# Kernel tuning notes

Measured on AMD Instinct MI355X. Metric: run time of the kernel, lower is better.

## Reference

```python
import jax, jax.numpy as jnp
import numpy as np

COUNT_BINS = 8
BOUND = 3.0
MIN_BIN_WIDTH = 1e-3
MIN_BIN_HEIGHT = 1e-3
MIN_DERIVATIVE = 1e-3
EPS = 1e-6


def _made_masks(D, H1, H2, M):
    indeg = np.arange(1, D + 1)                     # input degrees 1..D
    h1 = np.arange(H1) % (D - 1) + 1                # hidden degrees in [1, D-1]
    h2 = np.arange(H2) % (D - 1) + 1
    outdeg = np.tile(indeg, M)                      # (M*D,), reshape-compatible with (M, D)
    m1 = (h1[:, None] >= indeg[None, :]).astype(np.float32)   # (H1, D)
    m2 = (h2[:, None] >= h1[None, :]).astype(np.float32)      # (H2, H1)
    m3 = (outdeg[:, None] > h2[None, :]).astype(np.float32)   # (M*D, H2)
    return jnp.asarray(m1), jnp.asarray(m2), jnp.asarray(m3)


def _rq_spline_forward(x, w, h, d):
    # x: (B, D); w, h: (B, D, K) simplex weights; d: (B, D, K-1) softplus'd interior derivatives
    K = w.shape[-1]
    left, right = -BOUND, BOUND

    widths = MIN_BIN_WIDTH + (1.0 - MIN_BIN_WIDTH * K) * w
    heights = MIN_BIN_HEIGHT + (1.0 - MIN_BIN_HEIGHT * K) * h
    derivs = MIN_DERIVATIVE + d
    ones = jnp.ones_like(derivs[..., :1])
    derivs = jnp.concatenate([ones, derivs, ones], -1)          # (B, D, K+1), boundary slope 1

    cw = jnp.cumsum(widths, -1)
    edge_l = jnp.full_like(cw[..., :1], left)
    edge_r = jnp.full_like(cw[..., :1], right)
    cumw = jnp.concatenate([edge_l, left + (right - left) * cw[..., :-1], edge_r], -1)  # (B, D, K+1)
    widths = cumw[..., 1:] - cumw[..., :-1]
    ch = jnp.cumsum(heights, -1)
    cumh = jnp.concatenate([edge_l, left + (right - left) * ch[..., :-1], edge_r], -1)
    heights = cumh[..., 1:] - cumh[..., :-1]

    inside = (x >= left) & (x <= right)
    xc = jnp.clip(x, left, right)
    # pyro: bin_idx = sum(x >= cumwidths + eps) - 1
    idx = jnp.sum((xc[..., None] >= (cumw + EPS)).astype(jnp.int32), -1) - 1
    idx = jnp.clip(idx, 0, K - 1)                               # (B, D)

    def g(t):
        return jnp.take_along_axis(t, idx[..., None], axis=-1)[..., 0]

    x_k, w_k = g(cumw), g(widths)
    y_k, h_k = g(cumh), g(heights)
    delta = h_k / w_k
    d_k, d_k1 = g(derivs), g(derivs[..., 1:])

    theta = (xc - x_k) / w_k
    tt = theta * (1.0 - theta)
    num = h_k * (delta * theta ** 2 + d_k * tt)
    den = delta + (d_k + d_k1 - 2.0 * delta) * tt
    y = y_k + num / den
    dnum = delta ** 2 * (d_k1 * theta ** 2 + 2.0 * delta * tt + d_k * (1.0 - theta) ** 2)
    ld = jnp.log(dnum) - 2.0 * jnp.log(den)
    return jnp.where(inside, y, x), jnp.where(inside, ld, jnp.zeros_like(ld))


def _forward(x, W1, b1, W2, b2, W3, b3):
    B, D = x.shape
    H1, H2 = W1.shape[0], W2.shape[0]
    K = COUNT_BINS
    M = 3 * K - 1
    m1, m2, m3 = _made_masks(D, H1, H2, M)
    h1 = jax.nn.relu(x @ (W1 * m1).T + b1)
    h2 = jax.nn.relu(h1 @ (W2 * m2).T + b2)
    p = (h2 @ (W3 * m3).T + b3).reshape(B, M, D)                # (B, 3K-1, D)
    w = jax.nn.softmax(jnp.swapaxes(p[:, :K, :], 1, 2), axis=-1)          # (B, D, K)
    hgt = jax.nn.softmax(jnp.swapaxes(p[:, K:2 * K, :], 1, 2), axis=-1)   # (B, D, K)
    d = jax.nn.softplus(jnp.swapaxes(p[:, 2 * K:, :], 1, 2))              # (B, D, K-1)
    z, ld = _rq_spline_forward(x, w, hgt, d)
    return z, ld.sum(-1)


def setup_inputs() -> dict:
    key = jax.random.key(0)
    ks = jax.random.split(key, 7)
    B, D, H1, H2 = 32768, 64, 64, 32
    M = 3 * COUNT_BINS - 1
    s1, s2, s3 = 1.0 / np.sqrt(D), 1.0 / np.sqrt(H1), 1.0 / np.sqrt(H2)
    return {
        "x": jax.random.normal(ks[0], (B, D), jnp.float32),
        "W1": jax.random.uniform(ks[1], (H1, D), jnp.float32, -s1, s1),
        "b1": jax.random.uniform(ks[2], (H1,), jnp.float32, -s1, s1),
        "W2": jax.random.uniform(ks[3], (H2, H1), jnp.float32, -s2, s2),
        "b2": jax.random.uniform(ks[4], (H2,), jnp.float32, -s2, s2),
        "W3": jax.random.uniform(ks[5], (M * D, H2), jnp.float32, -s3, s3),
        "b3": jax.random.uniform(ks[6], (M * D,), jnp.float32, -s3, s3),
    }


def reference(x, W1, b1, W2, b2, W3, b3):
    return _forward(x, W1, b1, W2, b2, W3, b3)
```

## Files before the change

kernel.cpp:

```cpp
#include <hip/hip_runtime.h>

#define NM 23

typedef short short8 __attribute__((ext_vector_type(8)));
typedef float f32x4 __attribute__((ext_vector_type(4)));

#define LOG2E 1.44269504088896340736f

__device__ __forceinline__ float softplus_f(float v) {
  return fmaxf(v, 0.f) + __logf(1.f + __expf(-fabsf(v)));
}

__device__ __forceinline__ float fastrcp(float v) {
  return __builtin_amdgcn_rcpf(v);
}

__device__ __forceinline__ unsigned short bf16_rne(float x) {
  unsigned u = __float_as_uint(x);
  u += 0x7FFFu + ((u >> 16) & 1u);
  return (unsigned short)(u >> 16);
}

__global__ __launch_bounds__(256) void prep_kernel(
    const float* __restrict__ W1, const float* __restrict__ W2,
    const float* __restrict__ W3,
    unsigned short* __restrict__ B1hi, unsigned short* __restrict__ B1lo,
    unsigned short* __restrict__ B2hi, unsigned short* __restrict__ B2lo,
    unsigned short* __restrict__ B3hi, unsigned short* __restrict__ B3lo) {
  const int idx = blockIdx.x * 256 + threadIdx.x;
  const int j = idx & 7, lane = (idx >> 3) & 63;
  const int col = lane & 15, quad = lane >> 4;

  if (idx < 4096) {
    const int rest = idx >> 9, kt = rest & 1, nt = rest >> 1;
    const int k = kt * 32 + quad * 8 + j;
    const int n = nt * 16 + col;
    const float v = ((n % 63) >= k) ? W1[n * 64 + k] : 0.f;
    const unsigned short h = bf16_rne(v);
    B1hi[idx] = h;
    B1lo[idx] = bf16_rne(v - __uint_as_float(((unsigned)h) << 16));
  }
  if (idx < 2048) {
    const int rest = idx >> 9, kt = rest & 1, nt = rest >> 1;
    const int k = kt * 32 + quad * 8 + j;
    const int n = nt * 16 + col;
    const float v = ((k % 63) <= n) ? W2[n * 64 + k] : 0.f;
    const unsigned short h = bf16_rne(v);
    B2hi[idx] = h;
    B2lo[idx] = bf16_rne(v - __uint_as_float(((unsigned)h) << 16));
  }
  if (idx < 92 * 64 * 8) {
    const int nt = idx >> 9;
    const int n = nt * 16 + col;
    const int d = n & 63;
    const int m = n >> 6;
    const int k = quad * 8 + j;
    float v = (k < d) ? W3[(size_t)n * 32 + k] : 0.f;
    if (m < 16) v *= LOG2E;
    const unsigned short h = bf16_rne(v);
    B3hi[idx] = h;
    B3lo[idx] = bf16_rne(v - __uint_as_float(((unsigned)h) << 16));
  }
}

__device__ __forceinline__ void cvt_hilo(const float* src, short8& hi,
                                         short8& lo) {
  const f32x4 a0 = *reinterpret_cast<const f32x4*>(src);
  const f32x4 a1 = *reinterpret_cast<const f32x4*>(src + 4);
  const float af[8] = {a0.x, a0.y, a0.z, a0.w, a1.x, a1.y, a1.z, a1.w};
  #pragma unroll
  for (int j = 0; j < 8; ++j) {
    const unsigned short h = bf16_rne(af[j]);
    hi[j] = (short)h;
    lo[j] = (short)bf16_rne(af[j] - __uint_as_float(((unsigned)h) << 16));
  }
}

__global__ __launch_bounds__(512, 4) void fused_kernel(
    const float* __restrict__ x,
    const unsigned short* __restrict__ B1hi,
    const unsigned short* __restrict__ B1lo,
    const float* __restrict__ b1,
    const unsigned short* __restrict__ B2hi,
    const unsigned short* __restrict__ B2lo,
    const float* __restrict__ b2,
    const unsigned short* __restrict__ B3hi,
    const unsigned short* __restrict__ B3lo,
    const float* __restrict__ b3,
    float* __restrict__ out, int B) {
  __shared__ float h1s[32][68];
  __shared__ float h2s[32][68];
  __shared__ float b3s[64 * NM];
  __shared__ float ldp[4][32];

  const int t = threadIdx.x;
  const int b0 = blockIdx.x * 32;

  for (int idx = t; idx < 64 * NM; idx += 512) {
    const int dl = idx / NM, m = idx - dl * NM;
    const float s = (m < 16) ? LOG2E : 1.f;
    b3s[idx] = b3[m * 64 + dl] * s;
  }
  __syncthreads();

  const int lane = t & 63;
  const int wv   = __builtin_amdgcn_readfirstlane(t >> 6);
  const int col  = lane & 15;
  const int quad = lane >> 4;

  {
    const int mt1 = wv >> 2, nt1 = wv & 3;
    const float* xrow = x + (size_t)(b0 + mt1 * 16 + col) * 64;
    short8 ahi[2], alo[2];
    #pragma unroll
    for (int kt = 0; kt < 2; ++kt)
      cvt_hilo(xrow + kt * 32 + quad * 8, ahi[kt], alo[kt]);

    const float bv = b1[nt1 * 16 + col];
    f32x4 acc = {bv, bv, bv, bv};
    #pragma unroll
    for (int kt = 0; kt < 2; ++kt) {
      const size_t off = ((size_t)(nt1 * 2 + kt) * 64 + lane) * 8;
      const short8 bh = *reinterpret_cast<const short8*>(B1hi + off);
      const short8 bl = *reinterpret_cast<const short8*>(B1lo + off);
      acc = __builtin_amdgcn_mfma_f32_16x16x32_bf16(ahi[kt], bh, acc, 0, 0, 0);
      acc = __builtin_amdgcn_mfma_f32_16x16x32_bf16(alo[kt], bh, acc, 0, 0, 0);
      acc = __builtin_amdgcn_mfma_f32_16x16x32_bf16(ahi[kt], bl, acc, 0, 0, 0);
    }
    #pragma unroll
    for (int reg = 0; reg < 4; ++reg)
      h1s[mt1 * 16 + quad * 4 + reg][nt1 * 16 + col] = fmaxf(acc[reg], 0.f);
  }
  __syncthreads();

  if (wv < 4) {
    const int mt2 = wv >> 1, nt2 = wv & 1;
    short8 ahi[2], alo[2];
    #pragma unroll
    for (int kt = 0; kt < 2; ++kt)
      cvt_hilo(&h1s[mt2 * 16 + col][kt * 32 + quad * 8], ahi[kt], alo[kt]);

    const float bv = b2[nt2 * 16 + col];
    f32x4 acc = {bv, bv, bv, bv};
    #pragma unroll
    for (int kt = 0; kt < 2; ++kt) {
      const size_t off = ((size_t)(nt2 * 2 + kt) * 64 + lane) * 8;
      const short8 bh = *reinterpret_cast<const short8*>(B2hi + off);
      const short8 bl = *reinterpret_cast<const short8*>(B2lo + off);
      acc = __builtin_amdgcn_mfma_f32_16x16x32_bf16(ahi[kt], bh, acc, 0, 0, 0);
      acc = __builtin_amdgcn_mfma_f32_16x16x32_bf16(alo[kt], bh, acc, 0, 0, 0);
      acc = __builtin_amdgcn_mfma_f32_16x16x32_bf16(ahi[kt], bl, acc, 0, 0, 0);
    }
    #pragma unroll
    for (int reg = 0; reg < 4; ++reg)
      h2s[mt2 * 16 + quad * 4 + reg][nt2 * 16 + col] = fmaxf(acc[reg], 0.f);
  }
  __syncthreads();

  const int mt = wv >> 2, dc = wv & 3;
  const int row0 = mt * 16 + quad * 4;
  const int d = dc * 16 + col;

  short8 ahi, alo;
  cvt_hilo(&h2s[mt * 16 + col][quad * 8], ahi, alo);

  float xvv[4];
  #pragma unroll
  for (int reg = 0; reg < 4; ++reg)
    xvv[reg] = x[(size_t)(b0 + row0 + reg) * 64 + d];

  __syncthreads();

  float ldr[4] = {0.f, 0.f, 0.f, 0.f};
  const float WSC = 1.0f - 1e-3f * 8.0f;

  float xcv[4], fidx[4], xkv[4], wkv[4], ykv[4], hkv[4];

  {
    f32x4 acc[8];
    #pragma unroll
    for (int m = 0; m < 8; ++m) {
      const float bv = b3s[d * NM + m];
      acc[m] = (f32x4){bv, bv, bv, bv};
    }
    #pragma unroll
    for (int m = 0; m < 8; ++m) {
      const size_t off = ((size_t)(4 * m + dc) * 64 + lane) * 8;
      const short8 bh = *reinterpret_cast<const short8*>(B3hi + off);
      const short8 bl = *reinterpret_cast<const short8*>(B3lo + off);
      acc[m] = __builtin_amdgcn_mfma_f32_16x16x32_bf16(ahi, bh, acc[m], 0, 0, 0);
      acc[m] = __builtin_amdgcn_mfma_f32_16x16x32_bf16(alo, bh, acc[m], 0, 0, 0);
      acc[m] = __builtin_amdgcn_mfma_f32_16x16x32_bf16(ahi, bl, acc[m], 0, 0, 0);
    }
    #pragma unroll
    for (int reg = 0; reg < 4; ++reg) {
      float ew[8], sw = 0.f;
      #pragma unroll
      for (int k = 0; k < 8; ++k) { ew[k] = exp2f(acc[k][reg]); sw += ew[k]; }
      const float invw = fastrcp(sw);
      float cumw[9];
      cumw[0] = -3.f;
      float cw = 0.f;
      #pragma unroll
      for (int k = 0; k < 7; ++k) {
        cw += 1e-3f + WSC * (ew[k] * invw);
        cumw[k + 1] = fmaf(6.f, cw, -3.f);
      }
      cumw[8] = 3.f;

      const float xv = xvv[reg];
      const float xc = fminf(fmaxf(xv, -3.f), 3.f);
      float fi = 0.f, xk = cumw[0], xk1 = cumw[1];
      #pragma unroll
      for (int k = 1; k < 8; ++k) {
        const bool s = xc >= cumw[k] + 1e-6f;
        xk  = s ? cumw[k]     : xk;
        xk1 = s ? cumw[k + 1] : xk1;
        fi  = s ? (float)k    : fi;
      }
      xcv[reg] = xc; fidx[reg] = fi; xkv[reg] = xk; wkv[reg] = xk1 - xk;
    }
  }

  {
    f32x4 acc[8];
    #pragma unroll
    for (int m = 0; m < 8; ++m) {
      const float bv = b3s[d * NM + (8 + m)];
      acc[m] = (f32x4){bv, bv, bv, bv};
    }
    #pragma unroll
    for (int m = 0; m < 8; ++m) {
      const size_t off = ((size_t)(4 * (8 + m) + dc) * 64 + lane) * 8;
      const short8 bh = *reinterpret_cast<const short8*>(B3hi + off);
      const short8 bl = *reinterpret_cast<const short8*>(B3lo + off);
      acc[m] = __builtin_amdgcn_mfma_f32_16x16x32_bf16(ahi, bh, acc[m], 0, 0, 0);
      acc[m] = __builtin_amdgcn_mfma_f32_16x16x32_bf16(alo, bh, acc[m], 0, 0, 0);
      acc[m] = __builtin_amdgcn_mfma_f32_16x16x32_bf16(ahi, bl, acc[m], 0, 0, 0);
    }
    #pragma unroll
    for (int reg = 0; reg < 4; ++reg) {
      float eh[8], sh = 0.f;
      #pragma unroll
      for (int k = 0; k < 8; ++k) { eh[k] = exp2f(acc[k][reg]); sh += eh[k]; }
      const float invh = fastrcp(sh);
      float cumh[9];
      cumh[0] = -3.f;
      float ch = 0.f;
      #pragma unroll
      for (int k = 0; k < 7; ++k) {
        ch += 1e-3f + WSC * (eh[k] * invh);
        cumh[k + 1] = fmaf(6.f, ch, -3.f);
      }
      cumh[8] = 3.f;

      float yk = cumh[0], yk1 = cumh[1];
      #pragma unroll
      for (int k = 1; k < 8; ++k) {
        const bool s = fidx[reg] >= (float)k;
        yk  = s ? cumh[k]     : yk;
        yk1 = s ? cumh[k + 1] : yk1;
      }
      ykv[reg] = yk; hkv[reg] = yk1 - yk;
    }
  }

  {
    f32x4 acc[7];
    #pragma unroll
    for (int m = 0; m < 7; ++m) {
      const float bv = b3s[d * NM + (16 + m)];
      acc[m] = (f32x4){bv, bv, bv, bv};
    }
    #pragma unroll
    for (int m = 0; m < 7; ++m) {
      const size_t off = ((size_t)(4 * (16 + m) + dc) * 64 + lane) * 8;
      const short8 bh = *reinterpret_cast<const short8*>(B3hi + off);
      const short8 bl = *reinterpret_cast<const short8*>(B3lo + off);
      acc[m] = __builtin_amdgcn_mfma_f32_16x16x32_bf16(ahi, bh, acc[m], 0, 0, 0);
      acc[m] = __builtin_amdgcn_mfma_f32_16x16x32_bf16(alo, bh, acc[m], 0, 0, 0);
      acc[m] = __builtin_amdgcn_mfma_f32_16x16x32_bf16(ahi, bl, acc[m], 0, 0, 0);
    }
    #pragma unroll
    for (int reg = 0; reg < 4; ++reg) {
      float p[7];
      #pragma unroll
      for (int k = 0; k < 7; ++k) p[k] = acc[k][reg];
      const float fi = fidx[reg];

      float pa = p[0], pb = p[0];
      #pragma unroll
      for (int k = 2; k < 8; ++k) pa = (fi >= (float)k) ? p[k - 1] : pa;
      #pragma unroll
      for (int k = 1; k < 7; ++k) pb = (fi >= (float)k) ? p[k] : pb;
      const float spa = 1e-3f + softplus_f(pa);
      const float spb = 1e-3f + softplus_f(pb);
      const float dk  = (fi >= 0.5f) ? spa : 1.f;
      const float dk1 = (fi >= 6.5f) ? 1.f : spb;

      const float xc = xcv[reg], xk = xkv[reg], wk = wkv[reg];
      const float yk = ykv[reg], hk = hkv[reg];
      const float invwk = fastrcp(wk);
      const float delta = hk * invwk;
      const float theta = (xc - xk) * invwk;
      const float omt = 1.f - theta;
      const float tt = theta * omt;
      const float th2 = theta * theta;
      const float num = hk * (delta * th2 + dk * tt);
      const float den = delta + (dk + dk1 - 2.f * delta) * tt;
      const float rden = fastrcp(den);
      const float yv = yk + num * rden;
      const float dnum =
          delta * delta * (dk1 * th2 + 2.f * delta * tt + dk * omt * omt);
      const float ldv = __logf(dnum * rden * rden);

      const float xv = xvv[reg];
      const bool inside = (xv >= -3.f) && (xv <= 3.f);
      h2s[row0 + reg][d] = inside ? yv : xv;
      ldr[reg] += inside ? ldv : 0.f;
    }
  }

  #pragma unroll
  for (int mask = 1; mask <= 8; mask <<= 1) {
    #pragma unroll
    for (int reg = 0; reg < 4; ++reg)
      ldr[reg] += __shfl_xor(ldr[reg], mask, 64);
  }
  if (col == 0) {
    #pragma unroll
    for (int reg = 0; reg < 4; ++reg)
      ldp[dc][row0 + reg] = ldr[reg];
  }

  __syncthreads();

  if (t < 32)
    out[(size_t)B * 64 + b0 + t] =
        (ldp[0][t] + ldp[1][t]) + (ldp[2][t] + ldp[3][t]);

  {
    const int rr = t >> 4, c4 = (t & 15) * 4;
    const float4 v = make_float4(h2s[rr][c4 + 0], h2s[rr][c4 + 1],
                                 h2s[rr][c4 + 2], h2s[rr][c4 + 3]);
    *reinterpret_cast<float4*>(out + (size_t)(b0 + rr) * 64 + c4) = v;
  }
}

extern "C" void kernel_launch(void* const* d_in, const int* in_sizes, int n_in,
                              void* d_out, int out_size, void* d_ws, size_t ws_size,
                              hipStream_t stream) {
  const float* x  = (const float*)d_in[0];
  const float* W1 = (const float*)d_in[1];
  const float* b1 = (const float*)d_in[2];
  const float* W2 = (const float*)d_in[3];
  const float* b2 = (const float*)d_in[4];
  const float* W3 = (const float*)d_in[5];
  const float* b3 = (const float*)d_in[6];
  float* out = (float*)d_out;
  char* ws   = (char*)d_ws;

  unsigned short* B1hi = (unsigned short*)(ws);
  unsigned short* B1lo = (unsigned short*)(ws + 8192);
  unsigned short* B2hi = (unsigned short*)(ws + 16384);
  unsigned short* B2lo = (unsigned short*)(ws + 20480);
  unsigned short* B3hi = (unsigned short*)(ws + 24576);
  unsigned short* B3lo = (unsigned short*)(ws + 118784);

  const int B = in_sizes[0] / 64;

  prep_kernel<<<184, 256, 0, stream>>>(W1, W2, W3, B1hi, B1lo, B2hi, B2lo,
                                       B3hi, B3lo);

  fused_kernel<<<B / 32, 512, 0, stream>>>(
      x, B1hi, B1lo, b1, B2hi, B2lo, b2, B3hi, B3lo, b3, out, B);
}
```

Before: 106.3 us.

## Halve block tile to 16 rows and rewrite spline cumsum as scaled prefix

Each block now covers 16 batch rows with 256 threads (4 waves) instead of 32 rows with 512 threads. The per-wave MFMA tiling drops its M-tile index, and the shared buffers shrink to match. The width and height cumsums now accumulate raw exponentials and apply one fused scale plus a constant offset, instead of normalising and adding per step. Twice as many blocks is meant to improve scheduling granularity and latency hiding, but it repeats the b3 bias staging and weight fetches over fewer rows.

```diff
diff --git a/kernel.cpp b/kernel.cpp
--- a/kernel.cpp
+++ b/kernel.cpp
@@ -76,7 +76,7 @@
   }
 }
 
-__global__ __launch_bounds__(512, 4) void fused_kernel(
+__global__ __launch_bounds__(256, 4) void fused_kernel(
     const float* __restrict__ x,
     const unsigned short* __restrict__ B1hi,
     const unsigned short* __restrict__ B1lo,
@@ -88,15 +88,15 @@
     const unsigned short* __restrict__ B3lo,
     const float* __restrict__ b3,
     float* __restrict__ out, int B) {
-  __shared__ float h1s[32][68];
-  __shared__ float h2s[32][68];
+  __shared__ float h1s[16][68];
+  __shared__ float h2s[16][68];
   __shared__ float b3s[64 * NM];
-  __shared__ float ldp[4][32];
+  __shared__ float ldp[4][16];
 
   const int t = threadIdx.x;
-  const int b0 = blockIdx.x * 32;
-
-  for (int idx = t; idx < 64 * NM; idx += 512) {
+  const int b0 = blockIdx.x * 16;
+
+  for (int idx = t; idx < 64 * NM; idx += 256) {
     const int dl = idx / NM, m = idx - dl * NM;
     const float s = (m < 16) ? LOG2E : 1.f;
     b3s[idx] = b3[m * 64 + dl] * s;
@@ -109,8 +109,8 @@
   const int quad = lane >> 4;
 
   {
-    const int mt1 = wv >> 2, nt1 = wv & 3;
-    const float* xrow = x + (size_t)(b0 + mt1 * 16 + col) * 64;
+    const int nt1 = wv;
+    const float* xrow = x + (size_t)(b0 + col) * 64;
     short8 ahi[2], alo[2];
     #pragma unroll
     for (int kt = 0; kt < 2; ++kt)
@@ -129,16 +129,16 @@
     }
     #pragma unroll
     for (int reg = 0; reg < 4; ++reg)
-      h1s[mt1 * 16 + quad * 4 + reg][nt1 * 16 + col] = fmaxf(acc[reg], 0.f);
-  }
-  __syncthreads();
-
-  if (wv < 4) {
-    const int mt2 = wv >> 1, nt2 = wv & 1;
+      h1s[quad * 4 + reg][nt1 * 16 + col] = fmaxf(acc[reg], 0.f);
+  }
+  __syncthreads();
+
+  if (wv < 2) {
+    const int nt2 = wv;
     short8 ahi[2], alo[2];
     #pragma unroll
     for (int kt = 0; kt < 2; ++kt)
-      cvt_hilo(&h1s[mt2 * 16 + col][kt * 32 + quad * 8], ahi[kt], alo[kt]);
+      cvt_hilo(&h1s[col][kt * 32 + quad * 8], ahi[kt], alo[kt]);
 
     const float bv = b2[nt2 * 16 + col];
     f32x4 acc = {bv, bv, bv, bv};
@@ -153,16 +153,16 @@
     }
     #pragma unroll
     for (int reg = 0; reg < 4; ++reg)
-      h2s[mt2 * 16 + quad * 4 + reg][nt2 * 16 + col] = fmaxf(acc[reg], 0.f);
-  }
-  __syncthreads();
-
-  const int mt = wv >> 2, dc = wv & 3;
-  const int row0 = mt * 16 + quad * 4;
+      h2s[quad * 4 + reg][nt2 * 16 + col] = fmaxf(acc[reg], 0.f);
+  }
+  __syncthreads();
+
+  const int dc = wv;
+  const int row0 = quad * 4;
   const int d = dc * 16 + col;
 
   short8 ahi, alo;
-  cvt_hilo(&h2s[mt * 16 + col][quad * 8], ahi, alo);
+  cvt_hilo(&h2s[col][quad * 8], ahi, alo);
 
   float xvv[4];
   #pragma unroll
@@ -197,14 +197,15 @@
       float ew[8], sw = 0.f;
       #pragma unroll
       for (int k = 0; k < 8; ++k) { ew[k] = exp2f(acc[k][reg]); sw += ew[k]; }
-      const float invw = fastrcp(sw);
+      const float scale = 6.f * WSC * fastrcp(sw);
       float cumw[9];
       cumw[0] = -3.f;
-      float cw = 0.f;
+      float prefE = 0.f;
       #pragma unroll
       for (int k = 0; k < 7; ++k) {
-        cw += 1e-3f + WSC * (ew[k] * invw);
-        cumw[k + 1] = fmaf(6.f, cw, -3.f);
+        prefE += ew[k];
+        const float Ck = -3.f + 6e-3f * (float)(k + 1);
+        cumw[k + 1] = fmaf(prefE, scale, Ck);
       }
       cumw[8] = 3.f;
 
@@ -243,14 +244,15 @@
       float eh[8], sh = 0.f;
       #pragma unroll
       for (int k = 0; k < 8; ++k) { eh[k] = exp2f(acc[k][reg]); sh += eh[k]; }
-      const float invh = fastrcp(sh);
+      const float scale = 6.f * WSC * fastrcp(sh);
       float cumh[9];
       cumh[0] = -3.f;
-      float ch = 0.f;
+      float prefE = 0.f;
       #pragma unroll
       for (int k = 0; k < 7; ++k) {
-        ch += 1e-3f + WSC * (eh[k] * invh);
-        cumh[k + 1] = fmaf(6.f, ch, -3.f);
+        prefE += eh[k];
+        const float Ck = -3.f + 6e-3f * (float)(k + 1);
+        cumh[k + 1] = fmaf(prefE, scale, Ck);
       }
       cumh[8] = 3.f;
 
@@ -335,7 +337,7 @@
 
   __syncthreads();
 
-  if (t < 32)
+  if (t < 16)
     out[(size_t)B * 64 + b0 + t] =
         (ldp[0][t] + ldp[1][t]) + (ldp[2][t] + ldp[3][t]);
 
@@ -372,6 +374,6 @@
   prep_kernel<<<184, 256, 0, stream>>>(W1, W2, W3, B1hi, B1lo, B2hi, B2lo,
                                        B3hi, B3lo);
 
-  fused_kernel<<<B / 32, 512, 0, stream>>>(
+  fused_kernel<<<B / 16, 256, 0, stream>>>(
       x, B1hi, B1lo, b1, B2hi, B2lo, b2, B3hi, B3lo, b3, out, B);
 }
```

Result: slower. 109.2 us (+2.7%).
